# Kernel tuning notes

Measured on AMD Instinct MI355X. Metric: run time of the kernel, lower is better.

The kernel has to match this reference:

```python
import jax, jax.numpy as jnp
import numpy as np

N_NODES = 100000
N_EDGES = 3200000
D_IN = 128
D_HID = 32
D_OUT = 20
EPS = 1e-12  # matches torch F.normalize clamp


def setup_inputs() -> dict:
    key = jax.random.key(0)
    ks = jax.random.split(key, 10)
    x = jax.random.normal(ks[0], (N_NODES, D_IN), dtype=jnp.float32)
    edge_index = jax.random.randint(ks[1], (2, N_EDGES), 0, N_NODES, dtype=jnp.int32)
    def lin(k, fin, fout):
        return jax.random.normal(k, (fin, fout), dtype=jnp.float32) / np.float32(np.sqrt(fin))
    # SAGEConv: lin_l (applied to aggregated neighbors, has bias), lin_r (root, no bias)
    W1l = lin(ks[2], D_IN, D_HID); b1 = jnp.zeros((D_HID,), jnp.float32)
    W1r = lin(ks[3], D_IN, D_HID)
    W2l = lin(ks[4], D_HID, D_HID); b2 = jnp.zeros((D_HID,), jnp.float32)
    W2r = lin(ks[5], D_HID, D_HID)
    Wc = lin(ks[6], D_HID, D_OUT)
    bc = jax.random.normal(ks[7], (D_OUT,), dtype=jnp.float32) * 0.01
    return {"x": x, "edge_index": edge_index, "W1l": W1l, "b1": b1, "W1r": W1r,
            "W2l": W2l, "b2": b2, "W2r": W2r, "Wc": Wc, "bc": bc}


def _sage_conv(h, src, dst, Wl, bl, Wr):
    # mean aggregation of source features at destination nodes
    msgs = h[src]                                              # [E, d] gather
    agg = jax.ops.segment_sum(msgs, dst, num_segments=N_NODES)  # [N, d] scatter-add
    cnt = jax.ops.segment_sum(jnp.ones((src.shape[0],), h.dtype), dst, num_segments=N_NODES)
    mean = agg / jnp.maximum(cnt, 1.0)[:, None]
    out = mean @ Wl + bl + h @ Wr                              # combine neighbor + root
    norm = jnp.linalg.norm(out, axis=-1, keepdims=True)
    return out / jnp.maximum(norm, EPS)                        # L2 normalize


def reference(x, edge_index, W1l, b1, W1r, W2l, b2, W2r, Wc, bc):
    src, dst = edge_index[0], edge_index[1]
    h = jnp.tanh(_sage_conv(x, src, dst, W1l, b1, W1r))
    h = jnp.tanh(_sage_conv(h, src, dst, W2l, b2, W2r))
    out = jax.nn.log_softmax(h @ Wc + bc, axis=1)
    return (out, h)
```

## Files before the change

kernel.cpp:

```cpp
#include <hip/hip_runtime.h>
#include <hip/hip_fp16.h>
#include <cmath>

constexpr int NN   = 100000;
constexpr int NE   = 3200000;
constexpr int DIN  = 128;
constexpr int DH   = 32;
constexpr int DOUT = 20;

constexpr int NB    = 392;
constexpr int NBUSE = (NN + 255) / 256;
constexpr int NBLK  = 256;
constexpr int SLICE = NE / NBLK;

constexpr int NPB = 64;
constexpr int XSB = 136;
constexpr int HSS = 36;

typedef __attribute__((ext_vector_type(8))) short short8v;
typedef __attribute__((ext_vector_type(4))) float f32x4;

__device__ inline unsigned short f2bf(float f) {
    unsigned u = __builtin_bit_cast(unsigned, f);
    unsigned r = 0x7FFFu + ((u >> 16) & 1u);
    return (unsigned short)((u + r) >> 16);
}

__device__ inline unsigned f2fp8(float f) {
    unsigned u = __builtin_bit_cast(unsigned, f);
    unsigned s = (u >> 24) & 0x80u;
    unsigned au = u & 0x7fffffffu;
    if (au > 0x43E00000u) au = 0x43E00000u;
    unsigned u2 = au + 0x7FFFFu + ((au >> 20) & 1u);
    int em = (int)(u2 >> 20) - (120 << 3);
    em = em < 0 ? 0 : (em > 0x7E ? 0x7E : em);
    return s | (unsigned)em;
}
__device__ inline float dec8(unsigned b) {
    unsigned r = ((b & 0x80u) << 24) | (((b & 0x7fu) << 20) + 0x3C000000u);
    return __builtin_bit_cast(float, r);
}

__global__ __launch_bounds__(256, 4) void lin1_kernel(
    const float* __restrict__ x, const float* __restrict__ Wl,
    const float* __restrict__ Wr, unsigned char* __restrict__ xlf8,
    float* __restrict__ xr)
{
    __shared__ unsigned short xs[NPB * XSB];
    int t = threadIdx.x;
    int nodeBase = blockIdx.x * NPB;

    const float4* x4 = reinterpret_cast<const float4*>(x) + (size_t)nodeBase * (DIN / 4);
    for (int i = t; i < NPB * (DIN / 4); i += 256) {
        int n = i >> 5, c = i & 31;
        float4 v = make_float4(0.f, 0.f, 0.f, 0.f);
        if (nodeBase + n < NN) v = x4[i];
        unsigned lo = (unsigned)f2bf(v.x) | ((unsigned)f2bf(v.y) << 16);
        unsigned hi = (unsigned)f2bf(v.z) | ((unsigned)f2bf(v.w) << 16);
        *reinterpret_cast<uint2*>(&xs[n * XSB + c * 4]) = make_uint2(lo, hi);
    }
    __syncthreads();

    int wv   = t >> 6;
    int lane = t & 63;
    const float* W = (wv & 2) ? Wr : Wl;
    int jbase = (wv & 1) * 16;
    int ncol  = jbase + (lane & 15);
    int krow  = (lane >> 4) * 8;

    short8v bfrag[4];
#pragma unroll
    for (int ks = 0; ks < 4; ++ks) {
        const float* wp = W + (ks * 32 + krow) * DH + ncol;
        short8v f;
#pragma unroll
        for (int e = 0; e < 8; ++e) f[e] = (short)f2bf(wp[e * DH]);
        bfrag[ks] = f;
    }

    f32x4 acc[4];
#pragma unroll
    for (int m = 0; m < 4; ++m) acc[m] = f32x4{0.f, 0.f, 0.f, 0.f};

#pragma unroll
    for (int m = 0; m < 4; ++m) {
        int row = m * 16 + (lane & 15);
#pragma unroll
        for (int ks = 0; ks < 4; ++ks) {
            short8v a = *reinterpret_cast<const short8v*>(&xs[row * XSB + ks * 32 + krow]);
            acc[m] = __builtin_amdgcn_mfma_f32_16x16x32_bf16(a, bfrag[ks], acc[m], 0, 0, 0);
        }
    }

#pragma unroll
    for (int m = 0; m < 4; ++m) {
        int rbase = m * 16 + (lane >> 4) * 4;
#pragma unroll
        for (int r = 0; r < 4; ++r) {
            int node = nodeBase + rbase + r;
            if (node < NN) {
                float v = acc[m][r];
                if (wv & 2) xr[(size_t)node * DH + ncol] = v;
                else        xlf8[(size_t)node * DH + ncol] = (unsigned char)f2fp8(v);
            }
        }
    }
}

__global__ __launch_bounds__(1024) void countA_kernel(
    const int* __restrict__ ei, int* __restrict__ counts)
{
    __shared__ int h[NB];
    int blk = blockIdx.x, t = threadIdx.x;
    for (int i = t; i < NB; i += 1024) h[i] = 0;
    __syncthreads();
    int base = blk * SLICE;
    for (int i = base + t; i < base + SLICE; i += 1024) {
        int dst = ei[NE + i];
        atomicAdd(&h[dst >> 8], 1);
    }
    __syncthreads();
    for (int i = t; i < NB; i += 1024) counts[blk * NB + i] = h[i];
}

__global__ __launch_bounds__(256) void scanB1_kernel(
    const int* __restrict__ counts, int* __restrict__ offs, int* __restrict__ totals)
{
    __shared__ int sdata[256];
    int b = blockIdx.x, t = threadIdx.x;
    int v = counts[t * NB + b];
    int tp = (t & 7) * 32 + (t >> 3);
    sdata[tp] = v;
    __syncthreads();
    for (int off = 1; off < 256; off <<= 1) {
        int tmp = (t >= off) ? sdata[t - off] : 0;
        __syncthreads();
        sdata[t] += tmp;
        __syncthreads();
    }
    offs[b * 256 + t] = sdata[tp] - v;
    if (t == 255) totals[b] = sdata[255];
}

__global__ void scanB2_kernel(const int* __restrict__ totals, int* __restrict__ bases,
                              int* __restrict__ start)
{
    if (threadIdx.x == 0 && blockIdx.x == 0) {
        int acc = 0;
        for (int i = 0; i < NB; ++i) { bases[i] = acc; acc += totals[i]; }
        bases[NB] = acc;
        start[NN] = acc;
    }
}

__global__ __launch_bounds__(1024) void scatterC_kernel(
    const int* __restrict__ ei, const int* __restrict__ offs,
    const int* __restrict__ bases, unsigned* __restrict__ csrtmp)
{
    __shared__ int cnt[NB];
    __shared__ int wbase[NB];
    int blk = blockIdx.x, t = threadIdx.x;
    for (int i = t; i < NB; i += 1024) {
        cnt[i] = 0;
        wbase[i] = bases[i] + offs[i * 256 + blk];
    }
    __syncthreads();
    int base = blk * SLICE;
    for (int i = base + t; i < base + SLICE; i += 1024) {
        int dst = ei[NE + i];
        int src = ei[i];
        int b = dst >> 8;
        int r = atomicAdd(&cnt[b], 1);
        csrtmp[wbase[b] + r] = ((unsigned)(dst & 255) << 17) | (unsigned)src;
    }
}

__global__ __launch_bounds__(1024) void regroupD_kernel(
    const unsigned* __restrict__ csrtmp, const int* __restrict__ bases,
    int* __restrict__ csrsrc, int* __restrict__ start)
{
    __shared__ int h[256];
    __shared__ int sdata[256];
    int b = blockIdx.x, t = threadIdx.x;
    int lo = bases[b], hi = bases[b + 1];
    if (t < 256) h[t] = 0;
    __syncthreads();
    for (int i = lo + t; i < hi; i += 1024)
        atomicAdd(&h[csrtmp[i] >> 17], 1);
    __syncthreads();
    int v = 0;
    if (t < 256) { v = h[t]; sdata[t] = v; }
    __syncthreads();
    for (int off = 1; off < 256; off <<= 1) {
        int tmp = 0;
        if (t < 256 && t >= off) tmp = sdata[t - off];
        __syncthreads();
        if (t < 256) sdata[t] += tmp;
        __syncthreads();
    }
    if (t < 256) {
        int ex = sdata[t] - v;
        int node = b * 256 + t;
        if (node < NN) start[node] = lo + ex;
        h[t] = ex;
    }
    __syncthreads();
    for (int i = lo + t; i < hi; i += 1024) {
        unsigned u = csrtmp[i];
        int r = atomicAdd(&h[u >> 17], 1);
        csrsrc[lo + r] = (int)(u & 0x1FFFFu);
    }
}

__device__ inline float4 gather_core(const int* __restrict__ csrsrc,
                                     const unsigned* __restrict__ feat8,
                                     int s, int e, unsigned c)
{
    __half2 zero2 = __float2half2_rn(0.f);
    __half2 p0a = zero2, p0b = zero2, p1a = zero2, p1b = zero2;
    __half2 p2a = zero2, p2b = zero2, p3a = zero2, p3b = zero2;
    float4 corr = make_float4(0.f, 0.f, 0.f, 0.f);
    for (int i = s; i < e; i += 8) {
        unsigned off[8];
#pragma unroll
        for (int q = 0; q < 8; ++q) {
            int idx = i + q;
            idx = idx < e ? idx : e - 1;
            off[q] = (unsigned)csrsrc[idx] * 8u + c;
        }
        unsigned vv[8];
#pragma unroll
        for (int q = 0; q < 8; ++q) vv[q] = feat8[off[q]];
#pragma unroll
        for (int q = 0; q < 8; ++q) {
            unsigned w = vv[q];
            unsigned p01 = __builtin_amdgcn_perm(0u, w, 0x04010400u);
            unsigned p23 = __builtin_amdgcn_perm(0u, w, 0x04030402u);
            unsigned h01 = (p01 << 7) + ((p01 & 0x00800080u) << 7) + 0x20002000u;
            unsigned h23 = (p23 << 7) + ((p23 & 0x00800080u) << 7) + 0x20002000u;
            __half2 a01 = __builtin_bit_cast(__half2, h01);
            __half2 a23 = __builtin_bit_cast(__half2, h23);
            if ((q & 3) == 0) { p0a = __hadd2(p0a, a01); p0b = __hadd2(p0b, a23); }
            if ((q & 3) == 1) { p1a = __hadd2(p1a, a01); p1b = __hadd2(p1b, a23); }
            if ((q & 3) == 2) { p2a = __hadd2(p2a, a01); p2b = __hadd2(p2b, a23); }
            if ((q & 3) == 3) { p3a = __hadd2(p3a, a01); p3b = __hadd2(p3b, a23); }
        }
        if (i + 8 > e) {
            float k = (float)(i + 8 - e);
            unsigned w = vv[7];
            corr.x = k * dec8(w & 0xFFu);
            corr.y = k * dec8((w >> 8) & 0xFFu);
            corr.z = k * dec8((w >> 16) & 0xFFu);
            corr.w = k * dec8(w >> 24);
        }
    }
    float2 f0a = __half22float2(p0a), f1a = __half22float2(p1a);
    float2 f2a = __half22float2(p2a), f3a = __half22float2(p3a);
    float2 f0b = __half22float2(p0b), f1b = __half22float2(p1b);
    float2 f2b = __half22float2(p2b), f3b = __half22float2(p3b);
    float4 r;
    r.x = f0a.x + f1a.x + f2a.x + f3a.x - corr.x;
    r.y = f0a.y + f1a.y + f2a.y + f3a.y - corr.y;
    r.z = f0b.x + f1b.x + f2b.x + f3b.x - corr.z;
    r.w = f0b.y + f1b.y + f2b.y + f3b.y - corr.w;
    return r;
}

__global__ __launch_bounds__(256) void fused1_kernel(
    const int* __restrict__ start, const int* __restrict__ csrsrc,
    const unsigned* __restrict__ feat8, const float* __restrict__ xr,
    const float* __restrict__ b1, const float* __restrict__ W2l,
    const float* __restrict__ W2r, unsigned* __restrict__ hlf8u,
    float* __restrict__ hr)
{
    __shared__ float hs[32][HSS];
    int tid = blockIdx.x * 256 + threadIdx.x;
    int g = tid >> 3;
    unsigned c = threadIdx.x & 7;
    int nl = threadIdx.x >> 3;

    int s = start[g];
    int e = start[g + 1];
    float4 r = gather_core(csrsrc, feat8, s, e, c);

    float inv = 1.0f / fmaxf((float)(e - s), 1.0f);
    const float4 root = *reinterpret_cast<const float4*>(xr + (size_t)g * DH + c * 4);
    const float4 bb   = *reinterpret_cast<const float4*>(b1 + c * 4);
    float4 o;
    o.x = fmaf(r.x, inv, bb.x + root.x);
    o.y = fmaf(r.y, inv, bb.y + root.y);
    o.z = fmaf(r.z, inv, bb.z + root.z);
    o.w = fmaf(r.w, inv, bb.w + root.w);

    float ss = o.x*o.x + o.y*o.y + o.z*o.z + o.w*o.w;
    ss += __shfl_xor(ss, 1);
    ss += __shfl_xor(ss, 2);
    ss += __shfl_xor(ss, 4);
    float rn = 1.0f / fmaxf(sqrtf(ss), 1e-12f);
    float4 h;
    h.x = tanhf(o.x * rn); h.y = tanhf(o.y * rn);
    h.z = tanhf(o.z * rn); h.w = tanhf(o.w * rn);
    *reinterpret_cast<float4*>(&hs[nl][c * 4]) = h;

    float al[4] = {0.f, 0.f, 0.f, 0.f};
    float ar[4] = {0.f, 0.f, 0.f, 0.f};
#pragma unroll
    for (int k4 = 0; k4 < 8; ++k4) {
        float4 hv = *reinterpret_cast<const float4*>(&hs[nl][k4 * 4]);
        float hk[4] = {hv.x, hv.y, hv.z, hv.w};
#pragma unroll
        for (int kk = 0; kk < 4; ++kk) {
            const float4* wl4 = reinterpret_cast<const float4*>(W2l + (k4*4+kk) * DH + c * 4);
            const float4* wr4 = reinterpret_cast<const float4*>(W2r + (k4*4+kk) * DH + c * 4);
            float4 wl = wl4[0], wr = wr4[0];
            al[0] = fmaf(hk[kk], wl.x, al[0]);
            al[1] = fmaf(hk[kk], wl.y, al[1]);
            al[2] = fmaf(hk[kk], wl.z, al[2]);
            al[3] = fmaf(hk[kk], wl.w, al[3]);
            ar[0] = fmaf(hk[kk], wr.x, ar[0]);
            ar[1] = fmaf(hk[kk], wr.y, ar[1]);
            ar[2] = fmaf(hk[kk], wr.z, ar[2]);
            ar[3] = fmaf(hk[kk], wr.w, ar[3]);
        }
    }
    hlf8u[(size_t)g * 8 + c] = f2fp8(al[0]) | (f2fp8(al[1]) << 8) |
                               (f2fp8(al[2]) << 16) | (f2fp8(al[3]) << 24);
    *reinterpret_cast<float4*>(hr + (size_t)g * DH + c * 4) =
        make_float4(ar[0], ar[1], ar[2], ar[3]);
}

__global__ __launch_bounds__(256) void fused2_kernel(
    const int* __restrict__ start, const int* __restrict__ csrsrc,
    const unsigned* __restrict__ feat8, const float* __restrict__ hr,
    const float* __restrict__ b2, const float* __restrict__ Wc,
    const float* __restrict__ bc, float* __restrict__ h2out,
    float* __restrict__ outp)
{
    __shared__ float hs[32][HSS];
    int tid = blockIdx.x * 256 + threadIdx.x;
    int g = tid >> 3;
    unsigned c = threadIdx.x & 7;
    int nl = threadIdx.x >> 3;

    int s = start[g];
    int e = start[g + 1];
    float4 r = gather_core(csrsrc, feat8, s, e, c);

    float inv = 1.0f / fmaxf((float)(e - s), 1.0f);
    const float4 root = *reinterpret_cast<const float4*>(hr + (size_t)g * DH + c * 4);
    const float4 bb   = *reinterpret_cast<const float4*>(b2 + c * 4);
    float4 o;
    o.x = fmaf(r.x, inv, bb.x + root.x);
    o.y = fmaf(r.y, inv, bb.y + root.y);
    o.z = fmaf(r.z, inv, bb.z + root.z);
    o.w = fmaf(r.w, inv, bb.w + root.w);

    float ss = o.x*o.x + o.y*o.y + o.z*o.z + o.w*o.w;
    ss += __shfl_xor(ss, 1);
    ss += __shfl_xor(ss, 2);
    ss += __shfl_xor(ss, 4);
    float rn = 1.0f / fmaxf(sqrtf(ss), 1e-12f);
    float4 h;
    h.x = tanhf(o.x * rn); h.y = tanhf(o.y * rn);
    h.z = tanhf(o.z * rn); h.w = tanhf(o.w * rn);
    *reinterpret_cast<float4*>(&hs[nl][c * 4]) = h;
    *reinterpret_cast<float4*>(h2out + (size_t)g * DH + c * 4) = h;

    if (c < 4) {
        float z[5];
#pragma unroll
        for (int q = 0; q < 5; ++q) z[q] = bc[c * 5 + q];
#pragma unroll
        for (int k4 = 0; k4 < 8; ++k4) {
            float4 hv = *reinterpret_cast<const float4*>(&hs[nl][k4 * 4]);
            float hk[4] = {hv.x, hv.y, hv.z, hv.w};
#pragma unroll
            for (int kk = 0; kk < 4; ++kk) {
                const float* wc = Wc + (k4*4+kk) * DOUT + c * 5;
#pragma unroll
                for (int q = 0; q < 5; ++q) z[q] = fmaf(hk[kk], wc[q], z[q]);
            }
        }
        float m = z[0];
#pragma unroll
        for (int q = 1; q < 5; ++q) m = fmaxf(m, z[q]);
        m = fmaxf(m, __shfl_xor(m, 1));
        m = fmaxf(m, __shfl_xor(m, 2));
        float sum = 0.f;
#pragma unroll
        for (int q = 0; q < 5; ++q) sum += expf(z[q] - m);
        sum += __shfl_xor(sum, 1);
        sum += __shfl_xor(sum, 2);
        float lse = m + logf(sum);
        float* orow = outp + (size_t)g * DOUT + c * 5;
#pragma unroll
        for (int q = 0; q < 5; ++q) orow[q] = z[q] - lse;
    }
}

extern "C" void kernel_launch(void* const* d_in, const int* in_sizes, int n_in,
                              void* d_out, int out_size, void* d_ws, size_t ws_size,
                              hipStream_t stream) {
    const float* x   = (const float*)d_in[0];
    const int*   ei  = (const int*)d_in[1];
    const float* W1l = (const float*)d_in[2];
    const float* b1  = (const float*)d_in[3];
    const float* W1r = (const float*)d_in[4];
    const float* W2l = (const float*)d_in[5];
    const float* b2  = (const float*)d_in[6];
    const float* W2r = (const float*)d_in[7];
    const float* Wc  = (const float*)d_in[8];
    const float* bc  = (const float*)d_in[9];

    float* outp = (float*)d_out;
    float* hout = outp + (size_t)NN * DOUT;

    unsigned char* xlf8 = (unsigned char*)d_ws;
    unsigned char* hlf8 = xlf8 + (size_t)NN * DH;
    float* xr      = (float*)(hlf8 + (size_t)NN * DH);
    unsigned* csrtmp = (unsigned*)(xr + (size_t)NN * DH);
    int* csrsrc    = (int*)(csrtmp + NE);
    int* start     = csrsrc + NE;
    int* counts    = start + NN + 1;
    int* offs      = counts + NBLK * NB;
    int* totals    = offs + NB * NBLK;
    int* bases     = totals + NB;

    const int lin1Blocks  = (NN + NPB - 1) / NPB;
    const int fusedBlocks = (NN * 8) / 256;

    lin1_kernel<<<lin1Blocks, 256, 0, stream>>>(x, W1l, W1r, xlf8, xr);

    countA_kernel<<<NBLK, 1024, 0, stream>>>(ei, counts);
    scanB1_kernel<<<NB, 256, 0, stream>>>(counts, offs, totals);
    scanB2_kernel<<<1, 64, 0, stream>>>(totals, bases, start);
    scatterC_kernel<<<NBLK, 1024, 0, stream>>>(ei, offs, bases, csrtmp);
    regroupD_kernel<<<NBUSE, 1024, 0, stream>>>(csrtmp, bases, csrsrc, start);

    fused1_kernel<<<fusedBlocks, 256, 0, stream>>>(start, csrsrc,
        (const unsigned*)xlf8, xr, b1, W2l, W2r, (unsigned*)hlf8, xr);

    fused2_kernel<<<fusedBlocks, 256, 0, stream>>>(start, csrsrc,
        (const unsigned*)hlf8, xr, b2, Wc, bc, hout, outp);
}
```

Before: 168.1 us.

## Pad CSR rows to multiples of eight with a zero sentinel node for vector index loads

Each destination row in the CSR is padded to a multiple of eight entries, aligned per bucket, with padding that points at an extra sentinel node whose fp8 features are zeroed. The gather loop can then read indices as two int4 loads with no per-element clamping or tail correction. Degree is stored separately, and a constant bias for the padded zero-code entries is subtracted afterwards. This adds padding writes during CSR construction and some extra gather traffic on padded slots, and relies on fixed padding headroom and on the zero code decoding to a known constant.

Measured after the change: 171.0 us. About the same (+1.7%).

```diff
diff --git a/kernel.cpp b/kernel.cpp
--- a/kernel.cpp
+++ b/kernel.cpp
@@ -12,6 +12,8 @@
 constexpr int NBUSE = (NN + 255) / 256;
 constexpr int NBLK  = 256;
 constexpr int SLICE = NE / NBLK;
+constexpr int BPAD  = 1808;
+constexpr int CSRCAP = NE + NB * BPAD + 16;
 
 constexpr int NPB = 64;
 constexpr int XSB = 136;
@@ -143,13 +145,17 @@
 }
 
 __global__ void scanB2_kernel(const int* __restrict__ totals, int* __restrict__ bases,
-                              int* __restrict__ start)
-{
-    if (threadIdx.x == 0 && blockIdx.x == 0) {
+                              unsigned* __restrict__ xl8u, unsigned* __restrict__ hl8u)
+{
+    int t = threadIdx.x;
+    if (t == 0 && blockIdx.x == 0) {
         int acc = 0;
         for (int i = 0; i < NB; ++i) { bases[i] = acc; acc += totals[i]; }
         bases[NB] = acc;
-        start[NN] = acc;
+    }
+    if (blockIdx.x == 0 && t < 8) {
+        xl8u[(size_t)NN * 8 + t] = 0u;
+        hl8u[(size_t)NN * 8 + t] = 0u;
     }
 }
 
@@ -177,19 +183,20 @@
 
 __global__ __launch_bounds__(1024) void regroupD_kernel(
     const unsigned* __restrict__ csrtmp, const int* __restrict__ bases,
-    int* __restrict__ csrsrc, int* __restrict__ start)
+    int* __restrict__ csrsrc, int* __restrict__ start, int* __restrict__ deg)
 {
     __shared__ int h[256];
     __shared__ int sdata[256];
     int b = blockIdx.x, t = threadIdx.x;
     int lo = bases[b], hi = bases[b + 1];
+    int lopad = ((lo + 7) & ~7) + b * BPAD;
     if (t < 256) h[t] = 0;
     __syncthreads();
     for (int i = lo + t; i < hi; i += 1024)
         atomicAdd(&h[csrtmp[i] >> 17], 1);
     __syncthreads();
-    int v = 0;
-    if (t < 256) { v = h[t]; sdata[t] = v; }
+    int v = 0, pd = 0;
+    if (t < 256) { v = h[t]; pd = (v + 7) & ~7; sdata[t] = pd; }
     __syncthreads();
     for (int off = 1; off < 256; off <<= 1) {
         int tmp = 0;
@@ -199,38 +206,36 @@
         __syncthreads();
     }
     if (t < 256) {
-        int ex = sdata[t] - v;
+        int exPad = sdata[t] - pd;
         int node = b * 256 + t;
-        if (node < NN) start[node] = lo + ex;
-        h[t] = ex;
+        if (node < NN) { start[node] = lopad + exPad; deg[node] = v; }
+        h[t] = exPad;
+        for (int k = v; k < pd; ++k)
+            csrsrc[lopad + exPad + k] = NN;
     }
     __syncthreads();
     for (int i = lo + t; i < hi; i += 1024) {
         unsigned u = csrtmp[i];
         int r = atomicAdd(&h[u >> 17], 1);
-        csrsrc[lo + r] = (int)(u & 0x1FFFFu);
+        csrsrc[lopad + r] = (int)(u & 0x1FFFFu);
     }
 }
 
 __device__ inline float4 gather_core(const int* __restrict__ csrsrc,
                                      const unsigned* __restrict__ feat8,
-                                     int s, int e, unsigned c)
+                                     int s, int degPad, unsigned c)
 {
     __half2 zero2 = __float2half2_rn(0.f);
     __half2 p0a = zero2, p0b = zero2, p1a = zero2, p1b = zero2;
     __half2 p2a = zero2, p2b = zero2, p3a = zero2, p3b = zero2;
-    float4 corr = make_float4(0.f, 0.f, 0.f, 0.f);
-    for (int i = s; i < e; i += 8) {
-        unsigned off[8];
-#pragma unroll
-        for (int q = 0; q < 8; ++q) {
-            int idx = i + q;
-            idx = idx < e ? idx : e - 1;
-            off[q] = (unsigned)csrsrc[idx] * 8u + c;
-        }
+    const int4* cp = reinterpret_cast<const int4*>(csrsrc + s);
+    for (int i = 0; i < degPad; i += 8) {
+        int4 ca = cp[(i >> 2)];
+        int4 cb = cp[(i >> 2) + 1];
+        int sx[8] = {ca.x, ca.y, ca.z, ca.w, cb.x, cb.y, cb.z, cb.w};
         unsigned vv[8];
 #pragma unroll
-        for (int q = 0; q < 8; ++q) vv[q] = feat8[off[q]];
+        for (int q = 0; q < 8; ++q) vv[q] = feat8[(unsigned)sx[q] * 8u + c];
 #pragma unroll
         for (int q = 0; q < 8; ++q) {
             unsigned w = vv[q];
@@ -245,33 +250,25 @@
             if ((q & 3) == 2) { p2a = __hadd2(p2a, a01); p2b = __hadd2(p2b, a23); }
             if ((q & 3) == 3) { p3a = __hadd2(p3a, a01); p3b = __hadd2(p3b, a23); }
         }
-        if (i + 8 > e) {
-            float k = (float)(i + 8 - e);
-            unsigned w = vv[7];
-            corr.x = k * dec8(w & 0xFFu);
-            corr.y = k * dec8((w >> 8) & 0xFFu);
-            corr.z = k * dec8((w >> 16) & 0xFFu);
-            corr.w = k * dec8(w >> 24);
-        }
     }
     float2 f0a = __half22float2(p0a), f1a = __half22float2(p1a);
     float2 f2a = __half22float2(p2a), f3a = __half22float2(p3a);
     float2 f0b = __half22float2(p0b), f1b = __half22float2(p1b);
     float2 f2b = __half22float2(p2b), f3b = __half22float2(p3b);
     float4 r;
-    r.x = f0a.x + f1a.x + f2a.x + f3a.x - corr.x;
-    r.y = f0a.y + f1a.y + f2a.y + f3a.y - corr.y;
-    r.z = f0b.x + f1b.x + f2b.x + f3b.x - corr.z;
-    r.w = f0b.y + f1b.y + f2b.y + f3b.y - corr.w;
+    r.x = f0a.x + f1a.x + f2a.x + f3a.x;
+    r.y = f0a.y + f1a.y + f2a.y + f3a.y;
+    r.z = f0b.x + f1b.x + f2b.x + f3b.x;
+    r.w = f0b.y + f1b.y + f2b.y + f3b.y;
     return r;
 }
 
 __global__ __launch_bounds__(256) void fused1_kernel(
-    const int* __restrict__ start, const int* __restrict__ csrsrc,
-    const unsigned* __restrict__ feat8, const float* __restrict__ xr,
-    const float* __restrict__ b1, const float* __restrict__ W2l,
-    const float* __restrict__ W2r, unsigned* __restrict__ hlf8u,
-    float* __restrict__ hr)
+    const int* __restrict__ start, const int* __restrict__ deg,
+    const int* __restrict__ csrsrc, const unsigned* __restrict__ feat8,
+    const float* __restrict__ xr, const float* __restrict__ b1,
+    const float* __restrict__ W2l, const float* __restrict__ W2r,
+    unsigned* __restrict__ hlf8u, float* __restrict__ hr)
 {
     __shared__ float hs[32][HSS];
     int tid = blockIdx.x * 256 + threadIdx.x;
@@ -280,10 +277,13 @@
     int nl = threadIdx.x >> 3;
 
     int s = start[g];
-    int e = start[g + 1];
-    float4 r = gather_core(csrsrc, feat8, s, e, c);
-
-    float inv = 1.0f / fmaxf((float)(e - s), 1.0f);
+    int dg = deg[g];
+    int degPad = (dg + 7) & ~7;
+    float4 r = gather_core(csrsrc, feat8, s, degPad, c);
+    float pad = (float)(degPad - dg) * 0.0078125f;
+    r.x -= pad; r.y -= pad; r.z -= pad; r.w -= pad;
+
+    float inv = 1.0f / fmaxf((float)dg, 1.0f);
     const float4 root = *reinterpret_cast<const float4*>(xr + (size_t)g * DH + c * 4);
     const float4 bb   = *reinterpret_cast<const float4*>(b1 + c * 4);
     float4 o;
@@ -330,11 +330,11 @@
 }
 
 __global__ __launch_bounds__(256) void fused2_kernel(
-    const int* __restrict__ start, const int* __restrict__ csrsrc,
-    const unsigned* __restrict__ feat8, const float* __restrict__ hr,
-    const float* __restrict__ b2, const float* __restrict__ Wc,
-    const float* __restrict__ bc, float* __restrict__ h2out,
-    float* __restrict__ outp)
+    const int* __restrict__ start, const int* __restrict__ deg,
+    const int* __restrict__ csrsrc, const unsigned* __restrict__ feat8,
+    const float* __restrict__ hr, const float* __restrict__ b2,
+    const float* __restrict__ Wc, const float* __restrict__ bc,
+    float* __restrict__ h2out, float* __restrict__ outp)
 {
     __shared__ float hs[32][HSS];
     int tid = blockIdx.x * 256 + threadIdx.x;
@@ -343,10 +343,13 @@
     int nl = threadIdx.x >> 3;
 
     int s = start[g];
-    int e = start[g + 1];
-    float4 r = gather_core(csrsrc, feat8, s, e, c);
-
-    float inv = 1.0f / fmaxf((float)(e - s), 1.0f);
+    int dg = deg[g];
+    int degPad = (dg + 7) & ~7;
+    float4 r = gather_core(csrsrc, feat8, s, degPad, c);
+    float pad = (float)(degPad - dg) * 0.0078125f;
+    r.x -= pad; r.y -= pad; r.z -= pad; r.w -= pad;
+
+    float inv = 1.0f / fmaxf((float)dg, 1.0f);
     const float4 root = *reinterpret_cast<const float4*>(hr + (size_t)g * DH + c * 4);
     const float4 bb   = *reinterpret_cast<const float4*>(b2 + c * 4);
     float4 o;
@@ -416,12 +419,13 @@
     float* hout = outp + (size_t)NN * DOUT;
 
     unsigned char* xlf8 = (unsigned char*)d_ws;
-    unsigned char* hlf8 = xlf8 + (size_t)NN * DH;
-    float* xr      = (float*)(hlf8 + (size_t)NN * DH);
+    unsigned char* hlf8 = xlf8 + (size_t)(NN + 1) * DH;
+    float* xr      = (float*)(hlf8 + (size_t)(NN + 1) * DH);
     unsigned* csrtmp = (unsigned*)(xr + (size_t)NN * DH);
     int* csrsrc    = (int*)(csrtmp + NE);
-    int* start     = csrsrc + NE;
-    int* counts    = start + NN + 1;
+    int* start     = csrsrc + CSRCAP;
+    int* deg       = start + NN;
+    int* counts    = deg + NN;
     int* offs      = counts + NBLK * NB;
     int* totals    = offs + NB * NBLK;
     int* bases     = totals + NB;
@@ -433,13 +437,13 @@
 
     countA_kernel<<<NBLK, 1024, 0, stream>>>(ei, counts);
     scanB1_kernel<<<NB, 256, 0, stream>>>(counts, offs, totals);
-    scanB2_kernel<<<1, 64, 0, stream>>>(totals, bases, start);
+    scanB2_kernel<<<1, 64, 0, stream>>>(totals, bases, (unsigned*)xlf8, (unsigned*)hlf8);
     scatterC_kernel<<<NBLK, 1024, 0, stream>>>(ei, offs, bases, csrtmp);
-    regroupD_kernel<<<NBUSE, 1024, 0, stream>>>(csrtmp, bases, csrsrc, start);
-
-    fused1_kernel<<<fusedBlocks, 256, 0, stream>>>(start, csrsrc,
+    regroupD_kernel<<<NBUSE, 1024, 0, stream>>>(csrtmp, bases, csrsrc, start, deg);
+
+    fused1_kernel<<<fusedBlocks, 256, 0, stream>>>(start, deg, csrsrc,
         (const unsigned*)xlf8, xr, b1, W2l, W2r, (unsigned*)hlf8, xr);
 
-    fused2_kernel<<<fusedBlocks, 256, 0, stream>>>(start, csrsrc,
+    fused2_kernel<<<fusedBlocks, 256, 0, stream>>>(start, deg, csrsrc,
         (const unsigned*)hlf8, xr, b2, Wc, bc, hout, outp);
 }
```
